# Kernel tuning notes

Hardware: AMD Instinct MI355X
Metric: run time of the kernel (lower is better)

## Reference

```python
import jax, jax.numpy as jnp
import numpy as np
from jax import lax

B, S, N, DIM = 4, 512, 16, 8
D_MODEL, D_STATE = 1024, 64
INPUT_SIZE = N * DIM
LN_EPS = 1e-5


def setup_inputs() -> dict:
    key = jax.random.key(0)
    ks = jax.random.split(key, 8)
    s = 0.02
    x = jax.random.normal(ks[0], (B, S, N, DIM), dtype=jnp.float32)
    W_emb = jax.random.normal(ks[1], (INPUT_SIZE, D_MODEL), dtype=jnp.float32) * s
    b_emb = jnp.zeros((D_MODEL,), jnp.float32)
    W_xp = jax.random.normal(ks[2], (D_MODEL, 2 * D_STATE + 1), dtype=jnp.float32) * s
    b_xp = jnp.zeros((2 * D_STATE + 1,), jnp.float32)
    # A init: -exp(arange(1, d_state+1) * 0.1), matching the torch module
    A = -jnp.exp(jnp.arange(1, D_STATE + 1, dtype=jnp.float32) * 0.1)
    Dp = jnp.ones((D_MODEL,), jnp.float32)
    gamma = jnp.ones((D_MODEL,), jnp.float32)
    beta = jnp.zeros((D_MODEL,), jnp.float32)
    W_out = jax.random.normal(ks[3], (D_MODEL, INPUT_SIZE), dtype=jnp.float32) * s
    b_out = jnp.zeros((INPUT_SIZE,), jnp.float32)
    return {"x": x, "W_emb": W_emb, "b_emb": b_emb, "W_xp": W_xp, "b_xp": b_xp,
            "A": A, "Dp": Dp, "gamma": gamma, "beta": beta,
            "W_out": W_out, "b_out": b_out}


def reference(x, W_emb, b_emb, W_xp, b_xp, A, Dp, gamma, beta, W_out, b_out):
    b, s, n, dim = x.shape
    d_state = A.shape[0]
    d_model = W_emb.shape[1]
    u = x.reshape(b, s, n * dim) @ W_emb + b_emb            # [B,S,dm]
    sel = u @ W_xp + b_xp                                    # [B,S,2*ds+1]
    delta = jax.nn.softplus(sel[..., 0:1]) * 0.01            # [B,S,1]
    Bs = sel[..., 1:1 + d_state]                             # [B,S,ds]
    Cs = sel[..., 1 + d_state:]                              # [B,S,ds]
    A_bar = jnp.exp(delta * A)                               # [B,S,ds]
    B_bar = delta * Bs                                       # [B,S,ds]

    def step(h, inp):
        a_t, b_t, c_t, u_t = inp                             # [B,ds],[B,ds],[B,ds],[B,dm]
        h = h * a_t[:, None, :] + b_t[:, None, :] * u_t[:, :, None]  # [B,dm,ds]
        y_t = jnp.einsum('bmd,bd->bm', h, c_t) + u_t * Dp
        return h, y_t

    h0 = jnp.zeros((b, d_model, d_state), x.dtype)
    xs = (jnp.swapaxes(A_bar, 0, 1), jnp.swapaxes(B_bar, 0, 1),
          jnp.swapaxes(Cs, 0, 1), jnp.swapaxes(u, 0, 1))
    _, ys = lax.scan(step, h0, xs)                           # ys: [S,B,dm]
    y = jnp.swapaxes(ys, 0, 1)                               # [B,S,dm]
    mu = y.mean(-1, keepdims=True)
    var = y.var(-1, keepdims=True)
    yn = (y - mu) / jnp.sqrt(var + LN_EPS) * gamma + beta
    pred = yn @ W_out + b_out                                # [B,S,N*D]
    return pred.reshape(b, s, n, dim)
```

## Files before the change

kernel.cpp:

```cpp
#include <hip/hip_runtime.h>
#include <cstddef>

typedef __attribute__((ext_vector_type(8))) short short8;
typedef __attribute__((ext_vector_type(4))) float f32x4;

constexpr int ROWS = 2048;
constexpr int CL   = 32;

__device__ inline ushort tobf(float f) {
  union { float f; unsigned u; } v; v.f = f;
  return (ushort)((v.u + 0x7FFFu + ((v.u >> 16) & 1u)) >> 16);
}

__global__ __launch_bounds__(256)
void prep(const float* __restrict__ Wemb, const float* __restrict__ Wxp,
          const float* __restrict__ Wout, const float* __restrict__ x,
          ushort* __restrict__ WembT, ushort* __restrict__ wBCdT,
          ushort* __restrict__ WoutT, ushort* __restrict__ xbf) {
  int idx = blockIdx.x * 256 + threadIdx.x;
  if (idx < 131072) {
    int n = idx >> 7, k = idx & 127;
    WembT[idx] = tobf(Wemb[k * 1024 + n]);
  } else if (idx < 327680) {
    int j = idx - 131072;
    int n = j >> 10, k = j & 1023;
    float v = (n < 128) ? Wxp[k * 129 + 1 + n] : (n == 128 ? Wxp[k * 129] : 0.f);
    wBCdT[j] = tobf(v);
  } else if (idx < 458752) {
    int j = idx - 327680;
    int n = j >> 10, k = j & 1023;
    WoutT[j] = tobf(Wout[k * 128 + n]);
  } else if (idx < 720896) {
    int j = idx - 458752;
    xbf[j] = tobf(x[j]);
  }
}

template<bool SPLIT>
__global__ __launch_bounds__(256)
void gemm_bt_bf16(const ushort* __restrict__ A, const ushort* __restrict__ BT,
                  const float* __restrict__ bias, float* __restrict__ C,
                  ushort* __restrict__ Cbf, int M, int N, int K) {
  __shared__ __align__(16) ushort sA[8192];
  __shared__ __align__(16) ushort sB[8192];
  const int t  = threadIdx.x;
  const int n0 = blockIdx.x * 64;
  const int m0 = blockIdx.y * 64;
  const int kc = blockIdx.z << 7;

  #pragma unroll
  for (int i = 0; i < 4; ++i) {
    int c = t + (i << 8);
    int row = c >> 4, kk = (c & 15) << 3;
    float4 va = *(const float4*)(A  + (size_t)(m0 + row) * K + kc + kk);
    float4 vb = *(const float4*)(BT + (size_t)(n0 + row) * K + kc + kk);
    int byteoff = ((row << 8) + (kk << 1)) ^ ((row & 7) << 4);
    *(float4*)((char*)sA + byteoff) = va;
    *(float4*)((char*)sB + byteoff) = vb;
  }
  __syncthreads();

  const int lane = t & 63, w = t >> 6;
  const int wr = w << 4;
  const int colsel = lane & 15;
  const int kg = lane >> 4;

  short8 a[4];
  {
    int arow = wr + colsel;
    int lin = (arow << 8) + (kg << 4);
    int swz = (arow & 7) << 4;
    #pragma unroll
    for (int ks = 0; ks < 4; ++ks)
      a[ks] = *(const short8*)((const char*)sA + ((lin + (ks << 6)) ^ swz));
  }

  f32x4 acc[4];
  #pragma unroll
  for (int nf = 0; nf < 4; ++nf) acc[nf] = (f32x4)(0.f);

  #pragma unroll
  for (int nf = 0; nf < 4; ++nf) {
    int brow = (nf << 4) + colsel;
    int lin = (brow << 8) + (kg << 4);
    int swz = (brow & 7) << 4;
    #pragma unroll
    for (int ks = 0; ks < 4; ++ks) {
      short8 b = *(const short8*)((const char*)sB + ((lin + (ks << 6)) ^ swz));
      acc[nf] = __builtin_amdgcn_mfma_f32_16x16x32_bf16(a[ks], b, acc[nf], 0, 0, 0);
    }
  }

  const int r4 = kg << 2;
  float* Cp = C;
  if (SPLIT) Cp += (size_t)blockIdx.z * (size_t)M * N;
  #pragma unroll
  for (int nf = 0; nf < 4; ++nf) {
    int gn = n0 + (nf << 4) + colsel;
    #pragma unroll
    for (int reg = 0; reg < 4; ++reg) {
      int gm = m0 + wr + r4 + reg;
      if (SPLIT) {
        Cp[(size_t)gm * N + gn] = acc[nf][reg];
      } else {
        float v = acc[nf][reg] + bias[gn];
        C[(size_t)gm * N + gn] = v;
        Cbf[(size_t)gm * N + gn] = tobf(v);
      }
    }
  }
}

__global__ __launch_bounds__(256)
void k2e_epilogue(const float* __restrict__ part, const float* __restrict__ bxp,
                  const float* __restrict__ A, float* __restrict__ abc) {
  int gid = blockIdx.x * 256 + threadIdx.x;
  int row = gid >> 6, d = gid & 63;
  const size_t PN = (size_t)ROWS * 192;
  float sb = 0.f, sc = 0.f, dr = 0.f;
  #pragma unroll
  for (int z = 0; z < 8; ++z) {
    const float* p = part + z * PN + (size_t)row * 192;
    sb += p[d];
    sc += p[64 + d];
    dr += p[128];
  }
  sb += bxp[1 + d];
  sc += bxp[65 + d];
  float xv = dr + bxp[0];
  float sp = (xv > 15.f) ? xv : log1pf(__expf(xv));
  float delta = 0.01f * sp;
  float* o = abc + (size_t)row * 192;
  o[d]       = __expf(delta * A[d]);
  o[64 + d]  = delta * sb;
  o[128 + d] = sc;
}

__global__ __launch_bounds__(256)
void scan_sum(const float* __restrict__ u, const float* __restrict__ abc,
              float* __restrict__ cst, float* __restrict__ Ach) {
  __shared__ __align__(16) float sbuf[CL * 192];
  const int t = threadIdx.x, lane = t & 63, w = t >> 6;
  const int tc = blockIdx.x % 15;
  const int mg = (blockIdx.x / 15) & 3;
  const int b  = blockIdx.x / 60;
  const int r0 = b * 512 + tc * CL;

  const float4* src = (const float4*)(abc + (size_t)r0 * 192);
  #pragma unroll
  for (int i = 0; i < 6; ++i)
    ((float4*)sbuf)[t + i * 256] = src[t + i * 256];
  __syncthreads();

  const int m = (mg * 4 + w) * 64 + lane;
  const float* ub = u + (size_t)r0 * 1024 + m;
  const bool doAp = (mg == 0 && w == 0);

  float2 h[32];
  float2 ap[32];
  #pragma unroll
  for (int j = 0; j < 32; ++j) { h[j] = make_float2(0.f, 0.f); ap[j] = make_float2(1.f, 1.f); }

  float u0 = ub[0];
  float u1 = ub[1024];
  for (int s = 0; s < CL; ++s) {
    int sn = (s < CL - 3) ? s + 2 : CL - 1;
    float u2 = ub[(size_t)sn * 1024];
    const float* L = sbuf + s * 192;
    #pragma unroll
    for (int jj = 0; jj < 16; ++jj) {
      float4 a4 = *(const float4*)&L[4 * jj];
      float4 b4 = *(const float4*)&L[64 + 4 * jj];
      h[2 * jj].x     = fmaf(h[2 * jj].x,     a4.x, b4.x * u0);
      h[2 * jj].y     = fmaf(h[2 * jj].y,     a4.y, b4.y * u0);
      h[2 * jj + 1].x = fmaf(h[2 * jj + 1].x, a4.z, b4.z * u0);
      h[2 * jj + 1].y = fmaf(h[2 * jj + 1].y, a4.w, b4.w * u0);
    }
    if (doAp) {
      #pragma unroll
      for (int jj = 0; jj < 16; ++jj) {
        float4 a4 = *(const float4*)&L[4 * jj];
        ap[2 * jj].x     *= a4.x;
        ap[2 * jj].y     *= a4.y;
        ap[2 * jj + 1].x *= a4.z;
        ap[2 * jj + 1].y *= a4.w;
      }
    }
    u0 = u1; u1 = u2;
  }

  size_t cbase = (((size_t)b * 15 + tc) * 64) * 1024 + m;
  #pragma unroll
  for (int j = 0; j < 32; ++j) {
    cst[cbase + (size_t)(2 * j)     * 1024] = h[j].x;
    cst[cbase + (size_t)(2 * j + 1) * 1024] = h[j].y;
  }
  if (doAp && lane == 0) {
    float2* ad = (float2*)&Ach[((size_t)b * 15 + tc) * 64];
    #pragma unroll
    for (int j = 0; j < 32; ++j) ad[j] = ap[j];
  }
}

__global__ __launch_bounds__(256)
void scan_comb(float* __restrict__ cst, const float* __restrict__ Ach) {
  int g = blockIdx.x * 256 + threadIdx.x;
  int b = g >> 16;
  int rem = g & 65535;
  int d = rem >> 10;
  int m = rem & 1023;
  float h = 0.f;
  for (int t2 = 0; t2 < 15; ++t2) {
    size_t idx = (((size_t)(b * 15 + t2)) * 64 + d) * 1024 + m;
    h = fmaf(Ach[(b * 15 + t2) * 64 + d], h, cst[idx]);
    cst[idx] = h;
  }
}

__global__ __launch_bounds__(256)
void scan_out(const float* __restrict__ u, const float* __restrict__ abc,
              const float* __restrict__ cst, const float* __restrict__ Dp,
              float* __restrict__ y) {
  __shared__ __align__(16) float sbuf[CL * 192];
  const int t = threadIdx.x, lane = t & 63, w = t >> 6;
  const int tc = blockIdx.x & 15;
  const int mg = (blockIdx.x >> 4) & 3;
  const int b  = blockIdx.x >> 6;
  const int r0 = b * 512 + tc * CL;

  const float4* src = (const float4*)(abc + (size_t)r0 * 192);
  #pragma unroll
  for (int i = 0; i < 6; ++i)
    ((float4*)sbuf)[t + i * 256] = src[t + i * 256];
  __syncthreads();

  const int m = (mg * 4 + w) * 64 + lane;
  const float* ub = u + (size_t)r0 * 1024 + m;
  float*       yb = y + (size_t)r0 * 1024 + m;
  const float dp = Dp[m];

  float2 h[32];
  if (tc == 0) {
    #pragma unroll
    for (int j = 0; j < 32; ++j) h[j] = make_float2(0.f, 0.f);
  } else {
    size_t cbase = (((size_t)b * 15 + (tc - 1)) * 64) * 1024 + m;
    #pragma unroll
    for (int j = 0; j < 32; ++j) {
      h[j].x = cst[cbase + (size_t)(2 * j)     * 1024];
      h[j].y = cst[cbase + (size_t)(2 * j + 1) * 1024];
    }
  }

  float u0 = ub[0];
  float u1 = ub[1024];
  for (int s = 0; s < CL; ++s) {
    int sn = (s < CL - 3) ? s + 2 : CL - 1;
    float u2 = ub[(size_t)sn * 1024];
    const float* L = sbuf + s * 192;
    float y0 = 0.f, y1 = 0.f, y2 = 0.f, y3 = 0.f;
    #pragma unroll
    for (int jj = 0; jj < 16; ++jj) {
      float4 a4 = *(const float4*)&L[4 * jj];
      float4 b4 = *(const float4*)&L[64 + 4 * jj];
      float4 c4 = *(const float4*)&L[128 + 4 * jj];
      h[2 * jj].x     = fmaf(h[2 * jj].x,     a4.x, b4.x * u0);
      h[2 * jj].y     = fmaf(h[2 * jj].y,     a4.y, b4.y * u0);
      h[2 * jj + 1].x = fmaf(h[2 * jj + 1].x, a4.z, b4.z * u0);
      h[2 * jj + 1].y = fmaf(h[2 * jj + 1].y, a4.w, b4.w * u0);
      y0 = fmaf(c4.x, h[2 * jj].x,     y0);
      y1 = fmaf(c4.y, h[2 * jj].y,     y1);
      y2 = fmaf(c4.z, h[2 * jj + 1].x, y2);
      y3 = fmaf(c4.w, h[2 * jj + 1].y, y3);
    }
    yb[(size_t)s * 1024] = (y0 + y1) + (y2 + y3) + u0 * dp;
    u0 = u1; u1 = u2;
  }
}

__global__ __launch_bounds__(256)
void k4a_ln(const float* __restrict__ y, const float* __restrict__ gamma,
            const float* __restrict__ beta, ushort* __restrict__ ynbf) {
  __shared__ float red[8];
  int t = threadIdx.x, lane = t & 63, wv = t >> 6;
  int row = blockIdx.x;
  float4 v = *(const float4*)&y[(size_t)row * 1024 + t * 4];
  float s1 = v.x + v.y + v.z + v.w;
  float s2 = v.x * v.x + v.y * v.y + v.z * v.z + v.w * v.w;
  #pragma unroll
  for (int o = 32; o; o >>= 1) {
    s1 += __shfl_xor(s1, o, 64);
    s2 += __shfl_xor(s2, o, 64);
  }
  if (lane == 0) { red[wv] = s1; red[4 + wv] = s2; }
  __syncthreads();
  float S1 = red[0] + red[1] + red[2] + red[3];
  float S2 = red[4] + red[5] + red[6] + red[7];
  float mean = S1 * (1.f / 1024.f);
  float var  = S2 * (1.f / 1024.f) - mean * mean;
  float rstd = rsqrtf(var + 1e-5f);
  float4 g  = *(const float4*)&gamma[t * 4];
  float4 be = *(const float4*)&beta[t * 4];
  ushort4 o;
  o.x = tobf((v.x - mean) * rstd * g.x + be.x);
  o.y = tobf((v.y - mean) * rstd * g.y + be.y);
  o.z = tobf((v.z - mean) * rstd * g.z + be.z);
  o.w = tobf((v.w - mean) * rstd * g.w + be.w);
  *(ushort4*)&ynbf[(size_t)row * 1024 + t * 4] = o;
}

__global__ __launch_bounds__(256)
void k4c_out(const float* __restrict__ part, const float* __restrict__ bout,
             float* __restrict__ out) {
  int g4 = blockIdx.x * 256 + threadIdx.x;
  size_t idx = (size_t)g4 * 4;
  const size_t PN = (size_t)ROWS * 128;
  float4 s = *(const float4*)&part[idx];
  #pragma unroll
  for (int z = 1; z < 8; ++z) {
    float4 p = *(const float4*)&part[z * PN + idx];
    s.x += p.x; s.y += p.y; s.z += p.z; s.w += p.w;
  }
  float4 bb = *(const float4*)&bout[idx & 127];
  s.x += bb.x; s.y += bb.y; s.z += bb.z; s.w += bb.w;
  *(float4*)&out[idx] = s;
}

extern "C" void kernel_launch(void* const* d_in, const int* in_sizes, int n_in,
                              void* d_out, int out_size, void* d_ws, size_t ws_size,
                              hipStream_t stream) {
  const float* x     = (const float*)d_in[0];
  const float* W_emb = (const float*)d_in[1];
  const float* b_emb = (const float*)d_in[2];
  const float* W_xp  = (const float*)d_in[3];
  const float* b_xp  = (const float*)d_in[4];
  const float* A     = (const float*)d_in[5];
  const float* Dp    = (const float*)d_in[6];
  const float* gamma = (const float*)d_in[7];
  const float* beta  = (const float*)d_in[8];
  const float* W_out = (const float*)d_in[9];
  const float* b_out = (const float*)d_in[10];
  float* out = (float*)d_out;
  float* ws  = (float*)d_ws;

  float* u    = ws;
  float* y    = u + 2097152;
  float* abc  = y + 2097152;
  float* part = abc + 393216;
  float* cst  = part + 3145728;
  float* Ach  = cst + 3932160;
  ushort* ubf   = (ushort*)(Ach + 4096);
  ushort* ynbf  = ubf + 2097152;
  ushort* xbf   = ynbf + 2097152;
  ushort* WembT = xbf + 262144;
  ushort* wBCdT = WembT + 131072;
  ushort* WoutT = wBCdT + 196608;

  prep<<<2816, 256, 0, stream>>>(W_emb, W_xp, W_out, x, WembT, wBCdT, WoutT, xbf);
  gemm_bt_bf16<false><<<dim3(16, 32, 1), 256, 0, stream>>>(
      xbf, WembT, b_emb, u, ubf, 2048, 1024, 128);
  gemm_bt_bf16<true><<<dim3(3, 32, 8), 256, 0, stream>>>(
      ubf, wBCdT, nullptr, part, nullptr, 2048, 192, 1024);
  k2e_epilogue<<<512, 256, 0, stream>>>(part, b_xp, A, abc);
  scan_sum<<<240, 256, 0, stream>>>(u, abc, cst, Ach);
  scan_comb<<<1024, 256, 0, stream>>>(cst, Ach);
  scan_out<<<256, 256, 0, stream>>>(u, abc, cst, Dp, y);
  k4a_ln<<<2048, 256, 0, stream>>>(y, gamma, beta, ynbf);
  gemm_bt_bf16<true><<<dim3(2, 32, 8), 256, 0, stream>>>(
      ynbf, WoutT, nullptr, part, nullptr, 2048, 128, 1024);
  k4c_out<<<256, 256, 0, stream>>>(part, b_out, out);
}
```

Measured before the change: 156.6 us.

## Replace split-K partial buffers with atomics and fuse epilogues into scan and LN kernels

The split-K GEMMs now accumulate with atomicAdd into bias-initialized outputs (sel prefilled in prep, out prefilled in the LN kernel), and each block loops over two K-chunks instead of one. This removes the k2e_epilogue and k4c_out reduction kernels and the large partial buffers. The softplus/exp/delta transform is recomputed inside each scan kernel's shared-memory tile. The scans read u as bf16 instead of fp32, halving that traffic. The costs are atomic contention, nondeterministic summation order, and a lower-precision u in the recurrence.

```diff
diff --git a/kernel.cpp b/kernel.cpp
--- a/kernel.cpp
+++ b/kernel.cpp
@@ -4,19 +4,23 @@
 typedef __attribute__((ext_vector_type(8))) short short8;
 typedef __attribute__((ext_vector_type(4))) float f32x4;
 
-constexpr int ROWS = 2048;
-constexpr int CL   = 32;
+constexpr int CL = 32;
 
 __device__ inline ushort tobf(float f) {
   union { float f; unsigned u; } v; v.f = f;
   return (ushort)((v.u + 0x7FFFu + ((v.u >> 16) & 1u)) >> 16);
 }
+__device__ inline float frombf(ushort u) {
+  union { unsigned u; float f; } v; v.u = ((unsigned)u) << 16; return v.f;
+}
 
 __global__ __launch_bounds__(256)
 void prep(const float* __restrict__ Wemb, const float* __restrict__ Wxp,
           const float* __restrict__ Wout, const float* __restrict__ x,
+          const float* __restrict__ bxp,
           ushort* __restrict__ WembT, ushort* __restrict__ wBCdT,
-          ushort* __restrict__ WoutT, ushort* __restrict__ xbf) {
+          ushort* __restrict__ WoutT, ushort* __restrict__ xbf,
+          float* __restrict__ sel) {
   int idx = blockIdx.x * 256 + threadIdx.x;
   if (idx < 131072) {
     int n = idx >> 7, k = idx & 127;
@@ -33,111 +37,101 @@
   } else if (idx < 720896) {
     int j = idx - 458752;
     xbf[j] = tobf(x[j]);
-  }
-}
-
-template<bool SPLIT>
-__global__ __launch_bounds__(256)
-void gemm_bt_bf16(const ushort* __restrict__ A, const ushort* __restrict__ BT,
-                  const float* __restrict__ bias, float* __restrict__ C,
-                  ushort* __restrict__ Cbf, int M, int N, int K) {
+  } else if (idx < 1114112) {
+    int j = idx - 720896;
+    int c = j % 192;
+    sel[j] = (c < 128) ? bxp[1 + c] : (c == 128 ? bxp[0] : 0.f);
+  }
+}
+
+template<int MODE>
+__global__ __launch_bounds__(256)
+void gemm_bt(const ushort* __restrict__ A, const ushort* __restrict__ BT,
+             const float* __restrict__ bias, float* __restrict__ Cf,
+             ushort* __restrict__ Cbf, int M, int N, int K, int kchunk) {
   __shared__ __align__(16) ushort sA[8192];
   __shared__ __align__(16) ushort sB[8192];
   const int t  = threadIdx.x;
   const int n0 = blockIdx.x * 64;
   const int m0 = blockIdx.y * 64;
-  const int kc = blockIdx.z << 7;
-
-  #pragma unroll
-  for (int i = 0; i < 4; ++i) {
-    int c = t + (i << 8);
-    int row = c >> 4, kk = (c & 15) << 3;
-    float4 va = *(const float4*)(A  + (size_t)(m0 + row) * K + kc + kk);
-    float4 vb = *(const float4*)(BT + (size_t)(n0 + row) * K + kc + kk);
-    int byteoff = ((row << 8) + (kk << 1)) ^ ((row & 7) << 4);
-    *(float4*)((char*)sA + byteoff) = va;
-    *(float4*)((char*)sB + byteoff) = vb;
-  }
-  __syncthreads();
+  const int k0 = (MODE == 1) ? blockIdx.z * kchunk : 0;
+  const int k1 = (MODE == 1) ? k0 + kchunk : K;
 
   const int lane = t & 63, w = t >> 6;
   const int wr = w << 4;
   const int colsel = lane & 15;
   const int kg = lane >> 4;
 
-  short8 a[4];
-  {
-    int arow = wr + colsel;
-    int lin = (arow << 8) + (kg << 4);
-    int swz = (arow & 7) << 4;
-    #pragma unroll
-    for (int ks = 0; ks < 4; ++ks)
-      a[ks] = *(const short8*)((const char*)sA + ((lin + (ks << 6)) ^ swz));
-  }
-
   f32x4 acc[4];
   #pragma unroll
   for (int nf = 0; nf < 4; ++nf) acc[nf] = (f32x4)(0.f);
 
-  #pragma unroll
-  for (int nf = 0; nf < 4; ++nf) {
-    int brow = (nf << 4) + colsel;
-    int lin = (brow << 8) + (kg << 4);
-    int swz = (brow & 7) << 4;
-    #pragma unroll
-    for (int ks = 0; ks < 4; ++ks) {
-      short8 b = *(const short8*)((const char*)sB + ((lin + (ks << 6)) ^ swz));
-      acc[nf] = __builtin_amdgcn_mfma_f32_16x16x32_bf16(a[ks], b, acc[nf], 0, 0, 0);
-    }
-  }
-
+  for (int kc = k0; kc < k1; kc += 128) {
+    __syncthreads();
+    #pragma unroll
+    for (int i = 0; i < 4; ++i) {
+      int c = t + (i << 8);
+      int row = c >> 4, kk = (c & 15) << 3;
+      float4 va  = *(const float4*)(A  + (size_t)(m0 + row) * K + kc + kk);
+      float4 vb4 = *(const float4*)(BT + (size_t)(n0 + row) * K + kc + kk);
+      int byteoff = ((row << 8) + (kk << 1)) ^ ((row & 7) << 4);
+      *(float4*)((char*)sA + byteoff) = va;
+      *(float4*)((char*)sB + byteoff) = vb4;
+    }
+    __syncthreads();
+    short8 a[4];
+    {
+      int arow = wr + colsel;
+      int lin = (arow << 8) + (kg << 4);
+      int swz = (arow & 7) << 4;
+      #pragma unroll
+      for (int ks = 0; ks < 4; ++ks)
+        a[ks] = *(const short8*)((const char*)sA + ((lin + (ks << 6)) ^ swz));
+    }
+    #pragma unroll
+    for (int nf = 0; nf < 4; ++nf) {
+      int brow = (nf << 4) + colsel;
+      int lin = (brow << 8) + (kg << 4);
+      int swz = (brow & 7) << 4;
+      #pragma unroll
+      for (int ks = 0; ks < 4; ++ks) {
+        short8 b = *(const short8*)((const char*)sB + ((lin + (ks << 6)) ^ swz));
+        acc[nf] = __builtin_amdgcn_mfma_f32_16x16x32_bf16(a[ks], b, acc[nf], 0, 0, 0);
+      }
+    }
+  }
   const int r4 = kg << 2;
-  float* Cp = C;
-  if (SPLIT) Cp += (size_t)blockIdx.z * (size_t)M * N;
   #pragma unroll
   for (int nf = 0; nf < 4; ++nf) {
     int gn = n0 + (nf << 4) + colsel;
     #pragma unroll
     for (int reg = 0; reg < 4; ++reg) {
       int gm = m0 + wr + r4 + reg;
-      if (SPLIT) {
-        Cp[(size_t)gm * N + gn] = acc[nf][reg];
+      if (MODE == 0) {
+        Cbf[(size_t)gm * N + gn] = tobf(acc[nf][reg] + bias[gn]);
       } else {
-        float v = acc[nf][reg] + bias[gn];
-        C[(size_t)gm * N + gn] = v;
-        Cbf[(size_t)gm * N + gn] = tobf(v);
+        atomicAdd(&Cf[(size_t)gm * N + gn], acc[nf][reg]);
       }
     }
   }
 }
 
-__global__ __launch_bounds__(256)
-void k2e_epilogue(const float* __restrict__ part, const float* __restrict__ bxp,
-                  const float* __restrict__ A, float* __restrict__ abc) {
-  int gid = blockIdx.x * 256 + threadIdx.x;
-  int row = gid >> 6, d = gid & 63;
-  const size_t PN = (size_t)ROWS * 192;
-  float sb = 0.f, sc = 0.f, dr = 0.f;
-  #pragma unroll
-  for (int z = 0; z < 8; ++z) {
-    const float* p = part + z * PN + (size_t)row * 192;
-    sb += p[d];
-    sc += p[64 + d];
-    dr += p[128];
-  }
-  sb += bxp[1 + d];
-  sc += bxp[65 + d];
-  float xv = dr + bxp[0];
-  float sp = (xv > 15.f) ? xv : log1pf(__expf(xv));
-  float delta = 0.01f * sp;
-  float* o = abc + (size_t)row * 192;
-  o[d]       = __expf(delta * A[d]);
-  o[64 + d]  = delta * sb;
-  o[128 + d] = sc;
-}
-
-__global__ __launch_bounds__(256)
-void scan_sum(const float* __restrict__ u, const float* __restrict__ abc,
+__device__ __forceinline__ void transform_sbuf(float* sbuf, float a_d, int t) {
+  const int d = t & 63;
+  #pragma unroll
+  for (int i = 0; i < 8; ++i) {
+    float* R = sbuf + ((t >> 6) + i * 4) * 192;
+    float draw = R[128];
+    float sp = (draw > 15.f) ? draw : log1pf(__expf(draw));
+    float delta = 0.01f * sp;
+    R[d] = delta * R[d];
+    R[128 + d] = __expf(delta * a_d);
+  }
+}
+
+__global__ __launch_bounds__(256)
+void scan_sum(const ushort* __restrict__ ubf, const float* __restrict__ sel,
+              const float* __restrict__ A,
               float* __restrict__ cst, float* __restrict__ Ach) {
   __shared__ __align__(16) float sbuf[CL * 192];
   const int t = threadIdx.x, lane = t & 63, w = t >> 6;
@@ -146,31 +140,33 @@
   const int b  = blockIdx.x / 60;
   const int r0 = b * 512 + tc * CL;
 
-  const float4* src = (const float4*)(abc + (size_t)r0 * 192);
+  const float a_d = A[t & 63];
+  const float4* src = (const float4*)(sel + (size_t)r0 * 192);
   #pragma unroll
   for (int i = 0; i < 6; ++i)
     ((float4*)sbuf)[t + i * 256] = src[t + i * 256];
   __syncthreads();
+  transform_sbuf(sbuf, a_d, t);
+  __syncthreads();
 
   const int m = (mg * 4 + w) * 64 + lane;
-  const float* ub = u + (size_t)r0 * 1024 + m;
+  const ushort* ub = ubf + (size_t)r0 * 1024 + m;
   const bool doAp = (mg == 0 && w == 0);
 
-  float2 h[32];
-  float2 ap[32];
+  float2 h[32], ap[32];
   #pragma unroll
   for (int j = 0; j < 32; ++j) { h[j] = make_float2(0.f, 0.f); ap[j] = make_float2(1.f, 1.f); }
 
-  float u0 = ub[0];
-  float u1 = ub[1024];
+  float u0 = frombf(ub[0]);
+  float u1 = frombf(ub[1024]);
   for (int s = 0; s < CL; ++s) {
     int sn = (s < CL - 3) ? s + 2 : CL - 1;
-    float u2 = ub[(size_t)sn * 1024];
+    float u2 = frombf(ub[(size_t)sn * 1024]);
     const float* L = sbuf + s * 192;
     #pragma unroll
     for (int jj = 0; jj < 16; ++jj) {
-      float4 a4 = *(const float4*)&L[4 * jj];
-      float4 b4 = *(const float4*)&L[64 + 4 * jj];
+      float4 a4 = *(const float4*)&L[128 + 4 * jj];
+      float4 b4 = *(const float4*)&L[4 * jj];
       h[2 * jj].x     = fmaf(h[2 * jj].x,     a4.x, b4.x * u0);
       h[2 * jj].y     = fmaf(h[2 * jj].y,     a4.y, b4.y * u0);
       h[2 * jj + 1].x = fmaf(h[2 * jj + 1].x, a4.z, b4.z * u0);
@@ -179,7 +175,7 @@
     if (doAp) {
       #pragma unroll
       for (int jj = 0; jj < 16; ++jj) {
-        float4 a4 = *(const float4*)&L[4 * jj];
+        float4 a4 = *(const float4*)&L[128 + 4 * jj];
         ap[2 * jj].x     *= a4.x;
         ap[2 * jj].y     *= a4.y;
         ap[2 * jj + 1].x *= a4.z;
@@ -218,9 +214,9 @@
 }
 
 __global__ __launch_bounds__(256)
-void scan_out(const float* __restrict__ u, const float* __restrict__ abc,
-              const float* __restrict__ cst, const float* __restrict__ Dp,
-              float* __restrict__ y) {
+void scan_out(const ushort* __restrict__ ubf, const float* __restrict__ sel,
+              const float* __restrict__ A, const float* __restrict__ cst,
+              const float* __restrict__ Dp, float* __restrict__ y) {
   __shared__ __align__(16) float sbuf[CL * 192];
   const int t = threadIdx.x, lane = t & 63, w = t >> 6;
   const int tc = blockIdx.x & 15;
@@ -228,15 +224,18 @@
   const int b  = blockIdx.x >> 6;
   const int r0 = b * 512 + tc * CL;
 
-  const float4* src = (const float4*)(abc + (size_t)r0 * 192);
+  const float a_d = A[t & 63];
+  const float4* src = (const float4*)(sel + (size_t)r0 * 192);
   #pragma unroll
   for (int i = 0; i < 6; ++i)
     ((float4*)sbuf)[t + i * 256] = src[t + i * 256];
   __syncthreads();
+  transform_sbuf(sbuf, a_d, t);
+  __syncthreads();
 
   const int m = (mg * 4 + w) * 64 + lane;
-  const float* ub = u + (size_t)r0 * 1024 + m;
-  float*       yb = y + (size_t)r0 * 1024 + m;
+  const ushort* ub = ubf + (size_t)r0 * 1024 + m;
+  float* yb = y + (size_t)r0 * 1024 + m;
   const float dp = Dp[m];
 
   float2 h[32];
@@ -252,18 +251,18 @@
     }
   }
 
-  float u0 = ub[0];
-  float u1 = ub[1024];
+  float u0 = frombf(ub[0]);
+  float u1 = frombf(ub[1024]);
   for (int s = 0; s < CL; ++s) {
     int sn = (s < CL - 3) ? s + 2 : CL - 1;
-    float u2 = ub[(size_t)sn * 1024];
+    float u2 = frombf(ub[(size_t)sn * 1024]);
     const float* L = sbuf + s * 192;
     float y0 = 0.f, y1 = 0.f, y2 = 0.f, y3 = 0.f;
     #pragma unroll
     for (int jj = 0; jj < 16; ++jj) {
-      float4 a4 = *(const float4*)&L[4 * jj];
-      float4 b4 = *(const float4*)&L[64 + 4 * jj];
-      float4 c4 = *(const float4*)&L[128 + 4 * jj];
+      float4 a4 = *(const float4*)&L[128 + 4 * jj];
+      float4 b4 = *(const float4*)&L[4 * jj];
+      float4 c4 = *(const float4*)&L[64 + 4 * jj];
       h[2 * jj].x     = fmaf(h[2 * jj].x,     a4.x, b4.x * u0);
       h[2 * jj].y     = fmaf(h[2 * jj].y,     a4.y, b4.y * u0);
       h[2 * jj + 1].x = fmaf(h[2 * jj + 1].x, a4.z, b4.z * u0);
@@ -280,9 +279,12 @@
 
 __global__ __launch_bounds__(256)
 void k4a_ln(const float* __restrict__ y, const float* __restrict__ gamma,
-            const float* __restrict__ beta, ushort* __restrict__ ynbf) {
+            const float* __restrict__ beta, ushort* __restrict__ ynbf,
+            const float* __restrict__ bout, float* __restrict__ out) {
   __shared__ float red[8];
   int t = threadIdx.x, lane = t & 63, wv = t >> 6;
+  int gi = blockIdx.x * 256 + t;
+  if (gi < 262144) out[gi] = bout[gi & 127];
   int row = blockIdx.x;
   float4 v = *(const float4*)&y[(size_t)row * 1024 + t * 4];
   float s1 = v.x + v.y + v.z + v.w;
@@ -301,72 +303,52 @@
   float rstd = rsqrtf(var + 1e-5f);
   float4 g  = *(const float4*)&gamma[t * 4];
   float4 be = *(const float4*)&beta[t * 4];
-  ushort4 o;
-  o.x = tobf((v.x - mean) * rstd * g.x + be.x);
-  o.y = tobf((v.y - mean) * rstd * g.y + be.y);
-  o.z = tobf((v.z - mean) * rstd * g.z + be.z);
-  o.w = tobf((v.w - mean) * rstd * g.w + be.w);
-  *(ushort4*)&ynbf[(size_t)row * 1024 + t * 4] = o;
-}
-
-__global__ __launch_bounds__(256)
-void k4c_out(const float* __restrict__ part, const float* __restrict__ bout,
-             float* __restrict__ out) {
-  int g4 = blockIdx.x * 256 + threadIdx.x;
-  size_t idx = (size_t)g4 * 4;
-  const size_t PN = (size_t)ROWS * 128;
-  float4 s = *(const float4*)&part[idx];
-  #pragma unroll
-  for (int z = 1; z < 8; ++z) {
-    float4 p = *(const float4*)&part[z * PN + idx];
-    s.x += p.x; s.y += p.y; s.z += p.z; s.w += p.w;
-  }
-  float4 bb = *(const float4*)&bout[idx & 127];
-  s.x += bb.x; s.y += bb.y; s.z += bb.z; s.w += bb.w;
-  *(float4*)&out[idx] = s;
+  ushort4 o4;
+  o4.x = tobf((v.x - mean) * rstd * g.x + be.x);
+  o4.y = tobf((v.y - mean) * rstd * g.y + be.y);
+  o4.z = tobf((v.z - mean) * rstd * g.z + be.z);
+  o4.w = tobf((v.w - mean) * rstd * g.w + be.w);
+  *(ushort4*)&ynbf[(size_t)row * 1024 + t * 4] = o4;
 }
 
 extern "C" void kernel_launch(void* const* d_in, const int* in_sizes, int n_in,
                               void* d_out, int out_size, void* d_ws, size_t ws_size,
                               hipStream_t stream) {
   const float* x     = (const float*)d_in[0];
-  const float* W_emb = (const float*)d_in[1];
-  const float* b_emb = (const float*)d_in[2];
-  const float* W_xp  = (const float*)d_in[3];
-  const float* b_xp  = (const float*)d_in[4];
+  const float* Wemb  = (const float*)d_in[1];
+  const float* bemb  = (const float*)d_in[2];
+  const float* Wxp   = (const float*)d_in[3];
+  const float* bxp   = (const float*)d_in[4];
   const float* A     = (const float*)d_in[5];
   const float* Dp    = (const float*)d_in[6];
   const float* gamma = (const float*)d_in[7];
   const float* beta  = (const float*)d_in[8];
-  const float* W_out = (const float*)d_in[9];
-  const float* b_out = (const float*)d_in[10];
+  const float* Wout  = (const float*)d_in[9];
+  const float* bout  = (const float*)d_in[10];
   float* out = (float*)d_out;
   float* ws  = (float*)d_ws;
 
-  float* u    = ws;
-  float* y    = u + 2097152;
-  float* abc  = y + 2097152;
-  float* part = abc + 393216;
-  float* cst  = part + 3145728;
-  float* Ach  = cst + 3932160;
-  ushort* ubf   = (ushort*)(Ach + 4096);
+  float* sel = ws;
+  float* cst = ws + 393216;
+  float* y   = ws + 4325376;
+  float* Ach = ws + 6422528;
+  ushort* ubf   = (ushort*)(ws + 6426624);
   ushort* ynbf  = ubf + 2097152;
   ushort* xbf   = ynbf + 2097152;
   ushort* WembT = xbf + 262144;
   ushort* wBCdT = WembT + 131072;
   ushort* WoutT = wBCdT + 196608;
 
-  prep<<<2816, 256, 0, stream>>>(W_emb, W_xp, W_out, x, WembT, wBCdT, WoutT, xbf);
-  gemm_bt_bf16<false><<<dim3(16, 32, 1), 256, 0, stream>>>(
-      xbf, WembT, b_emb, u, ubf, 2048, 1024, 128);
-  gemm_bt_bf16<true><<<dim3(3, 32, 8), 256, 0, stream>>>(
-      ubf, wBCdT, nullptr, part, nullptr, 2048, 192, 1024);
-  k2e_epilogue<<<512, 256, 0, stream>>>(part, b_xp, A, abc);
-  scan_sum<<<240, 256, 0, stream>>>(u, abc, cst, Ach);
+  prep<<<4352, 256, 0, stream>>>(Wemb, Wxp, Wout, x, bxp,
+                                 WembT, wBCdT, WoutT, xbf, sel);
+  gemm_bt<0><<<dim3(16, 32, 1), 256, 0, stream>>>(
+      xbf, WembT, bemb, nullptr, ubf, 2048, 1024, 128, 0);
+  gemm_bt<1><<<dim3(3, 32, 4), 256, 0, stream>>>(
+      ubf, wBCdT, nullptr, sel, nullptr, 2048, 192, 1024, 256);
+  scan_sum<<<240, 256, 0, stream>>>(ubf, sel, A, cst, Ach);
   scan_comb<<<1024, 256, 0, stream>>>(cst, Ach);
-  scan_out<<<256, 256, 0, stream>>>(u, abc, cst, Dp, y);
-  k4a_ln<<<2048, 256, 0, stream>>>(y, gamma, beta, ynbf);
-  gemm_bt_bf16<true><<<dim3(2, 32, 8), 256, 0, stream>>>(
-      ynbf, WoutT, nullptr, part, nullptr, 2048, 128, 1024);
-  k4c_out<<<256, 256, 0, stream>>>(part, b_out, out);
-}
+  scan_out<<<256, 256, 0, stream>>>(ubf, sel, A, cst, Dp, y);
+  k4a_ln<<<2048, 256, 0, stream>>>(y, gamma, beta, ynbf, bout, out);
+  gemm_bt<1><<<dim3(2, 32, 4), 256, 0, stream>>>(
+      ynbf, WoutT, nullptr, out, nullptr, 2048, 128, 1024, 256);
+}
```

New measurement: 160.8 us. 2.7% more time.
